# Performance work log

Measured on AMD Instinct MI355X. Metric: run time of the kernel, lower is better.

The kernel has to match this reference:

```python
import jax, jax.numpy as jnp
import numpy as np

B, S, D = 1, 2048, 2048
H, KV, HD = 16, 4, 128
E, TOPK, F = 8, 2, 2048
THETA = 500000.0
CLIP = 8.0
EPS = 1e-5


def setup_inputs() -> dict:
    key = jax.random.key(0)
    ks = jax.random.split(key, 8)
    sc = 0.02
    return {
        "hidden_states": jax.random.normal(ks[0], (B, S, D), jnp.float32),
        "position_ids": jnp.arange(S, dtype=jnp.int64)[None, :].repeat(B, axis=0),
        "ln1_w": jnp.ones((D,), jnp.float32),
        "ln2_w": jnp.ones((D,), jnp.float32),
        "wqkv": jax.random.normal(ks[1], (D, (H + 2 * KV) * HD), jnp.float32) * sc,
        "wo": jax.random.normal(ks[2], (H * HD, D), jnp.float32) * sc,
        "router_w": jax.random.normal(ks[3], (E, D), jnp.float32) * sc,
        "w1": jax.random.normal(ks[4], (E, D, F), jnp.float32) * sc,
        "v1": jax.random.normal(ks[5], (E, D, F), jnp.float32) * sc,
        "w2": jax.random.normal(ks[6], (E, F, D), jnp.float32) * sc,
    }


def _layernorm(x, w):
    mu = jnp.mean(x, axis=-1, keepdims=True)
    var = jnp.mean((x - mu) ** 2, axis=-1, keepdims=True)
    return (x - mu) * jax.lax.rsqrt(var + EPS) * w


def _rotate_half(x):
    x1, x2 = jnp.split(x, 2, axis=-1)
    return jnp.concatenate([-x2, x1], axis=-1)


def _rope(pos):
    inv_freq = 1.0 / (THETA ** (jnp.arange(0, HD, 2, dtype=jnp.float32) / HD))
    ang = pos.astype(jnp.float32)[..., None] * inv_freq  # [B,S,HD/2]
    ang = jnp.concatenate([ang, ang], axis=-1)  # [B,S,HD]
    return jnp.cos(ang)[:, None], jnp.sin(ang)[:, None]  # [B,1,S,HD]


def _forward(hidden_states, position_ids, ln1_w, ln2_w, wqkv, wo, router_w, w1, v1, w2):
    x = hidden_states
    # --- attention sublayer ---
    h = _layernorm(x, ln1_w)
    qkv = jnp.clip(h @ wqkv, -CLIP, CLIP)  # [B,S,(H+2KV)*HD]
    q, k, v = jnp.split(qkv, [H * HD, (H + KV) * HD], axis=-1)
    q = q.reshape(B, S, H, HD).transpose(0, 2, 1, 3)   # [B,H,S,HD]
    k = k.reshape(B, S, KV, HD).transpose(0, 2, 1, 3)  # [B,KV,S,HD]
    v = v.reshape(B, S, KV, HD).transpose(0, 2, 1, 3)
    cos, sin = _rope(position_ids)
    q = q * cos + _rotate_half(q) * sin
    k = k * cos + _rotate_half(k) * sin
    rep = H // KV
    k = jnp.repeat(k, rep, axis=1)  # [B,H,S,HD]
    v = jnp.repeat(v, rep, axis=1)
    scores = jnp.einsum("bhqd,bhkd->bhqk", q, k) / np.sqrt(HD).astype(np.float32)
    causal = jnp.tril(jnp.ones((S, S), bool))
    scores = jnp.where(causal, scores, jnp.finfo(scores.dtype).min)
    probs = jax.nn.softmax(scores, axis=-1)
    attn = jnp.einsum("bhqk,bhkd->bhqd", probs, v)
    attn = attn.transpose(0, 2, 1, 3).reshape(B, S, H * HD) @ wo
    x = x + attn
    # --- MoE FFN sublayer ---
    h = _layernorm(x, ln2_w).reshape(B * S, D)  # [T,D]
    logits = h @ router_w.T                      # [T,E]
    rp = jax.nn.softmax(logits, axis=-1)
    top_w, top_i = jax.lax.top_k(rp, TOPK)       # [T,K]
    top_w = top_w / jnp.sum(top_w, axis=-1, keepdims=True)
    T = B * S
    gate = jnp.zeros((T, E), h.dtype).at[jnp.arange(T)[:, None], top_i].add(top_w)
    g = jax.nn.silu(jnp.einsum("td,edf->tef", h, w1)) * jnp.einsum("td,edf->tef", h, v1)
    y = jnp.einsum("tef,efd,te->td", g, w2, gate)
    x = x + y.reshape(B, S, D)
    return x


def reference(hidden_states, position_ids, ln1_w, ln2_w, wqkv, wo, router_w, w1, v1, w2):
    return _forward(hidden_states, position_ids, ln1_w, ln2_w, wqkv, wo, router_w, w1, v1, w2)
```

## Files before the change

kernel.cpp:

```cpp
#include <hip/hip_runtime.h>

#define S_LEN 2048
#define DMODEL 2048
#define NH 16
#define NKV 4
#define HD 128
#define NE 8
#define FF 2048
#define QKV_N 3072

typedef __attribute__((ext_vector_type(8))) short short8;
typedef __attribute__((ext_vector_type(4))) float f32x4;

__device__ inline unsigned short f2bf(float f) {
  unsigned int u = __builtin_bit_cast(unsigned int, f);
  u += 0x7fffu + ((u >> 16) & 1u);
  return (unsigned short)(u >> 16);
}
__device__ inline float bf2f(unsigned short h) {
  unsigned int u = ((unsigned int)h) << 16;
  return __builtin_bit_cast(float, u);
}
__device__ inline void split2(float v, unsigned short& h, unsigned short& l) {
  h = f2bf(v);
  l = f2bf(v - bf2f(h));
}


__device__ inline void gload16(const void* g, void* l) {
  __builtin_amdgcn_global_load_lds((const __attribute__((address_space(1))) unsigned int*)g,
                                   (__attribute__((address_space(3))) unsigned int*)l,
                                   16, 0, 0);
}
__device__ inline void stageB_chunk(const unsigned short* __restrict__ chunk,
                                    unsigned short* __restrict__ lds) {
  int w = threadIdx.x >> 6, l = threadIdx.x & 63;
  const unsigned short* s = chunk + w * 1024 + l * 8;
  unsigned short* d = lds + w * 1024;
  gload16(s, d);
  gload16(s + 512, d + 512);
}

#define WVM0   asm volatile("s_waitcnt vmcnt(0)" ::: "memory")
#define WVM4   asm volatile("s_waitcnt vmcnt(4)" ::: "memory")
#define WVM6   asm volatile("s_waitcnt vmcnt(6)" ::: "memory")
#define WVM8   asm volatile("s_waitcnt vmcnt(8)" ::: "memory")
#define WVM12  asm volatile("s_waitcnt vmcnt(12)" ::: "memory")
#define WAIT_ALL  asm volatile("s_waitcnt vmcnt(0) lgkmcnt(0)" ::: "memory")
#define WAIT_LDS  asm volatile("s_waitcnt lgkmcnt(0)" ::: "memory")
#define SCHEDBAR  __builtin_amdgcn_sched_barrier(0)
#define BAR       __builtin_amdgcn_s_barrier()


__device__ inline void mma16(const unsigned short* As, const unsigned short* Bs,
                             int wr, int wc, f32x4 acc[4][4]) {
  int l = threadIdx.x & 63;
  int lr = l & 15, lg = l >> 4;
  int qoff = ((lg ^ ((lr ^ (lr >> 2)) & 3)) << 3);
  short8 a[4], b[4];
#pragma unroll
  for (int m = 0; m < 4; m++)
    a[m] = *(const short8*)(As + (wr + m * 16 + lr) * 32 + qoff);
#pragma unroll
  for (int n = 0; n < 4; n++)
    b[n] = *(const short8*)(Bs + (wc + n * 16 + lr) * 32 + qoff);
#pragma unroll
  for (int m = 0; m < 4; m++)
#pragma unroll
    for (int n = 0; n < 4; n++)
      acc[m][n] = __builtin_amdgcn_mfma_f32_16x16x32_bf16(a[m], b[n], acc[m][n], 0, 0, 0);
}

__device__ inline void mma16_dualB(const unsigned short* As, const unsigned short* Bs1,
                                   const unsigned short* Bs2, int wr, int wc,
                                   f32x4 acc1[4][4], f32x4 acc2[4][4]) {
  int l = threadIdx.x & 63;
  int lr = l & 15, lg = l >> 4;
  int qoff = ((lg ^ ((lr ^ (lr >> 2)) & 3)) << 3);
  short8 a[4], b1[4], b2[4];
#pragma unroll
  for (int m = 0; m < 4; m++)
    a[m] = *(const short8*)(As + (wr + m * 16 + lr) * 32 + qoff);
#pragma unroll
  for (int n = 0; n < 4; n++) {
    b1[n] = *(const short8*)(Bs1 + (wc + n * 16 + lr) * 32 + qoff);
    b2[n] = *(const short8*)(Bs2 + (wc + n * 16 + lr) * 32 + qoff);
  }
#pragma unroll
  for (int m = 0; m < 4; m++)
#pragma unroll
    for (int n = 0; n < 4; n++) {
      acc1[m][n] = __builtin_amdgcn_mfma_f32_16x16x32_bf16(a[m], b1[n], acc1[m][n], 0, 0, 0);
      acc2[m][n] = __builtin_amdgcn_mfma_f32_16x16x32_bf16(a[m], b2[n], acc2[m][n], 0, 0, 0);
    }
}

__device__ inline void mma16_split_reg(const unsigned short* Ash, const unsigned short* Asl,
                                       const unsigned short* Bsh, const unsigned short* Bsl,
                                       int wr, int wc, f32x4 acc[4][4]) {
  int l = threadIdx.x & 63;
  int lr = l & 15, lg = l >> 4;
  int qoff = ((lg ^ ((lr ^ (lr >> 2)) & 3)) << 3);
  short8 ah[4], al[4], bh[4], bl[4];
#pragma unroll
  for (int m = 0; m < 4; m++) {
    ah[m] = *(const short8*)(Ash + (wr + m * 16 + lr) * 32 + qoff);
    al[m] = *(const short8*)(Asl + (wr + m * 16 + lr) * 32 + qoff);
  }
#pragma unroll
  for (int n = 0; n < 4; n++) {
    bh[n] = *(const short8*)(Bsh + (wc + n * 16 + lr) * 32 + qoff);
    bl[n] = *(const short8*)(Bsl + (wc + n * 16 + lr) * 32 + qoff);
  }
#pragma unroll
  for (int m = 0; m < 4; m++)
#pragma unroll
    for (int n = 0; n < 4; n++) {
      acc[m][n] = __builtin_amdgcn_mfma_f32_16x16x32_bf16(ah[m], bh[n], acc[m][n], 0, 0, 0);
      acc[m][n] = __builtin_amdgcn_mfma_f32_16x16x32_bf16(ah[m], bl[n], acc[m][n], 0, 0, 0);
      acc[m][n] = __builtin_amdgcn_mfma_f32_16x16x32_bf16(al[m], bh[n], acc[m][n], 0, 0, 0);
    }
}


__global__ __launch_bounds__(256) void k_pack1(const float* __restrict__ src, long ld,
                                               long zs, int nc,
                                               unsigned short* __restrict__ dst) {
  __shared__ float tile[32][132];
  const float* Sp = src + (long)blockIdx.z * zs;
  int c = blockIdx.x, t = threadIdx.x;
  for (int i = 0; i < 4; i++) {
    int kt = blockIdx.y * 4 + i;
    long k0 = (long)kt * 32, n0 = (long)c * 128;
    {
      int k = t >> 3, nn = (t & 7) * 16;
      const float4* p = (const float4*)(Sp + (k0 + k) * ld + n0 + nn);
#pragma unroll
      for (int j = 0; j < 4; j++) *(float4*)&tile[k][nn + j * 4] = p[j];
    }
    __syncthreads();
    size_t cbase = ((size_t)(blockIdx.z * nc + c) * 64 + kt) * 4096;
#pragma unroll
    for (int uu = 0; uu < 2; uu++) {
      int u = t * 2 + uu;
      int n = u >> 2, qp = u & 3;
      int q = qp ^ ((n ^ (n >> 2)) & 3);
      unsigned short hb[8] __attribute__((aligned(16)));
#pragma unroll
      for (int j = 0; j < 8; j++) hb[j] = f2bf(tile[8 * q + j][n]);
      *(uint4*)(dst + cbase + u * 8) = *(const uint4*)hb;
    }
    __syncthreads();
  }
}

__global__ __launch_bounds__(256) void k_pack2(const float* __restrict__ src, long ld,
                                               long zs, int nc,
                                               unsigned short* __restrict__ dh,
                                               unsigned short* __restrict__ dl) {
  __shared__ float tile[32][132];
  const float* Sp = src + (long)blockIdx.z * zs;
  int c = blockIdx.x, t = threadIdx.x;
  for (int i = 0; i < 4; i++) {
    int kt = blockIdx.y * 4 + i;
    long k0 = (long)kt * 32, n0 = (long)c * 128;
    {
      int k = t >> 3, nn = (t & 7) * 16;
      const float4* p = (const float4*)(Sp + (k0 + k) * ld + n0 + nn);
#pragma unroll
      for (int j = 0; j < 4; j++) *(float4*)&tile[k][nn + j * 4] = p[j];
    }
    __syncthreads();
    size_t cbase = ((size_t)(blockIdx.z * nc + c) * 64 + kt) * 4096;
#pragma unroll
    for (int uu = 0; uu < 2; uu++) {
      int u = t * 2 + uu;
      int n = u >> 2, qp = u & 3;
      int q = qp ^ ((n ^ (n >> 2)) & 3);
      unsigned short hb[8] __attribute__((aligned(16)));
      unsigned short lb[8] __attribute__((aligned(16)));
#pragma unroll
      for (int j = 0; j < 8; j++) split2(tile[8 * q + j][n], hb[j], lb[j]);
      *(uint4*)(dh + cbase + u * 8) = *(const uint4*)hb;
      *(uint4*)(dl + cbase + u * 8) = *(const uint4*)lb;
    }
    __syncthreads();
  }
}


__global__ __launch_bounds__(256) void k_qkv_s(const unsigned short* __restrict__ APh,
                                               const unsigned short* __restrict__ APl,
                                               const unsigned short* __restrict__ BPh,
                                               const unsigned short* __restrict__ BPl,
                                               float* __restrict__ C) {
  __shared__ unsigned short Ash[2 * 4096], Asl[2 * 4096], Bsh[2 * 4096], Bsl[2 * 4096];
  size_t ab = (size_t)blockIdx.y * 64 * 4096;
  size_t cb = (size_t)blockIdx.x * 64 * 4096;
  int w = threadIdx.x >> 6;
  int wr = (w >> 1) * 64, wc = (w & 1) * 64;
  stageB_chunk(APh + ab, Ash);
  stageB_chunk(APl + ab, Asl);
  stageB_chunk(BPh + cb, Bsh);
  stageB_chunk(BPl + cb, Bsl);
  WAIT_ALL;
  BAR;
  f32x4 acc[4][4] = {};
  for (int kt = 0; kt < 64; kt++) {
    int cur = (kt & 1) << 12, nxt = 4096 - cur;
    if (kt + 1 < 64) {
      size_t o = (size_t)(kt + 1) * 4096;
      stageB_chunk(APh + ab + o, Ash + nxt);
      stageB_chunk(APl + ab + o, Asl + nxt);
      stageB_chunk(BPh + cb + o, Bsh + nxt);
      stageB_chunk(BPl + cb + o, Bsl + nxt);
    }
    SCHEDBAR;
    mma16_split_reg(Ash + cur, Asl + cur, Bsh + cur, Bsl + cur, wr, wc, acc);
    SCHEDBAR;
    WAIT_ALL;
    BAR;
  }
  int row0 = blockIdx.y * 128, col0 = blockIdx.x * 128;
  int l = threadIdx.x & 63;
  int er = wr + ((l >> 4) << 2), ec = wc + (l & 15);
#pragma unroll
  for (int m = 0; m < 4; m++)
#pragma unroll
    for (int n = 0; n < 4; n++)
#pragma unroll
      for (int r = 0; r < 4; r++) {
        float v = acc[m][n][r];
        v = fminf(fmaxf(v, -8.f), 8.f);
        C[(size_t)(row0 + er + m * 16 + r) * QKV_N + col0 + ec + n * 16] = v;
      }
}

__global__ __launch_bounds__(256) void k_wo_s(const unsigned short* __restrict__ APh,
                                              const unsigned short* __restrict__ APl,
                                              const unsigned short* __restrict__ BPh,
                                              const unsigned short* __restrict__ BPl,
                                              const float* __restrict__ resid,
                                              float* __restrict__ x1) {
  __shared__ unsigned short Ash[2 * 4096], Asl[2 * 4096], Bsh[2 * 4096], Bsl[2 * 4096];
  size_t ab = (size_t)blockIdx.y * 64 * 4096;
  size_t cb = (size_t)blockIdx.x * 64 * 4096;
  int w = threadIdx.x >> 6;
  int wr = (w >> 1) * 64, wc = (w & 1) * 64;
  stageB_chunk(APh + ab, Ash);
  stageB_chunk(APl + ab, Asl);
  stageB_chunk(BPh + cb, Bsh);
  stageB_chunk(BPl + cb, Bsl);
  WAIT_ALL;
  BAR;
  f32x4 acc[4][4] = {};
  for (int kt = 0; kt < 64; kt++) {
    int cur = (kt & 1) << 12, nxt = 4096 - cur;
    if (kt + 1 < 64) {
      size_t o = (size_t)(kt + 1) * 4096;
      stageB_chunk(APh + ab + o, Ash + nxt);
      stageB_chunk(APl + ab + o, Asl + nxt);
      stageB_chunk(BPh + cb + o, Bsh + nxt);
      stageB_chunk(BPl + cb + o, Bsl + nxt);
    }
    SCHEDBAR;
    mma16_split_reg(Ash + cur, Asl + cur, Bsh + cur, Bsl + cur, wr, wc, acc);
    SCHEDBAR;
    WAIT_ALL;
    BAR;
  }
  int row0 = blockIdx.y * 128, col0 = blockIdx.x * 128;
  int l = threadIdx.x & 63;
  int er = wr + ((l >> 4) << 2), ec = wc + (l & 15);
#pragma unroll
  for (int m = 0; m < 4; m++)
#pragma unroll
    for (int n = 0; n < 4; n++)
#pragma unroll
      for (int r = 0; r < 4; r++) {
        size_t idx = (size_t)(row0 + er + m * 16 + r) * DMODEL + col0 + ec + n * 16;
        x1[idx] = resid[idx] + acc[m][n][r];
      }
}


__global__ __launch_bounds__(128) void k_flash(const unsigned short* __restrict__ qh,
                                               const unsigned short* __restrict__ ql,
                                               const unsigned short* __restrict__ kPh,
                                               const unsigned short* __restrict__ kPl,
                                               const unsigned short* __restrict__ vPh,
                                               const unsigned short* __restrict__ vPl,
                                               unsigned short* __restrict__ atPh,
                                               unsigned short* __restrict__ atPl) {
  int bid = blockIdx.x;
  int h = (bid & 7) | ((bid >> 8) << 3);
  int rt = (bid >> 3) & 31;
  int kv = h >> 2;
  int ntiles = (rt >> 1) + 1;
  __shared__ float Pds[2][32 * 132];
  int t = threadIdx.x;
  int w = t >> 6, l = t & 63;
  int lr = l & 15, lg = l >> 4;
  int qoff = ((lg ^ ((lr ^ (lr >> 2)) & 3)) << 3);
  int wrow0 = rt * 64 + w * 32;
  const unsigned short* Qbh = qh + (size_t)h * S_LEN * HD;
  const unsigned short* Qbl = ql + (size_t)h * S_LEN * HD;
  const unsigned short* Kch = kPh + (size_t)kv * 64 * 4096;
  const unsigned short* Kcl = kPl + (size_t)kv * 64 * 4096;
  const unsigned short* Vch = vPh + (size_t)kv * 64 * 4096;
  const unsigned short* Vcl = vPl + (size_t)kv * 64 * 4096;
  float* Pw = &Pds[w][0];
  float mrun[2][4], lrun[2][4];
  f32x4 Oc[2][8];
#pragma unroll
  for (int m = 0; m < 2; m++)
#pragma unroll
    for (int r = 0; r < 4; r++) { mrun[m][r] = -3.4e38f; lrun[m][r] = 0.f; }
#pragma unroll
  for (int m = 0; m < 2; m++)
#pragma unroll
    for (int n = 0; n < 8; n++)
#pragma unroll
      for (int r = 0; r < 4; r++) Oc[m][n][r] = 0.f;
  const float scale = 0.08838834764831845f;

  for (int kt = 0; kt < ntiles; kt++) {
    f32x4 Sa[2][8];
#pragma unroll
    for (int m = 0; m < 2; m++)
#pragma unroll
      for (int n = 0; n < 8; n++)
#pragma unroll
        for (int r = 0; r < 4; r++) Sa[m][n][r] = 0.f;
#pragma unroll
    for (int kst = 0; kst < 4; kst++) {
      short8 qfh[2], qfl[2];
#pragma unroll
      for (int m = 0; m < 2; m++) {
        size_t o = (size_t)(wrow0 + m * 16 + lr) * HD + kst * 32 + lg * 8;
        qfh[m] = *(const short8*)(Qbh + o);
        qfl[m] = *(const short8*)(Qbl + o);
      }
      const unsigned short* Kh = Kch + (size_t)(kt * 4 + kst) * 4096;
      const unsigned short* Kl = Kcl + (size_t)(kt * 4 + kst) * 4096;
      short8 bh[8], bl[8];
#pragma unroll
      for (int n = 0; n < 8; n++) {
        bh[n] = *(const short8*)(Kh + (n * 16 + lr) * 32 + qoff);
        bl[n] = *(const short8*)(Kl + (n * 16 + lr) * 32 + qoff);
      }
#pragma unroll
      for (int m = 0; m < 2; m++)
#pragma unroll
        for (int n = 0; n < 8; n++) {
          Sa[m][n] = __builtin_amdgcn_mfma_f32_16x16x32_bf16(qfh[m], bh[n], Sa[m][n], 0, 0, 0);
          Sa[m][n] = __builtin_amdgcn_mfma_f32_16x16x32_bf16(qfh[m], bl[n], Sa[m][n], 0, 0, 0);
          Sa[m][n] = __builtin_amdgcn_mfma_f32_16x16x32_bf16(qfl[m], bh[n], Sa[m][n], 0, 0, 0);
        }
    }
#pragma unroll
    for (int m = 0; m < 2; m++)
#pragma unroll
      for (int r = 0; r < 4; r++) {
        int row = wrow0 + m * 16 + lg * 4 + r;
        float mx = mrun[m][r];
#pragma unroll
        for (int n = 0; n < 8; n++) {
          float v = Sa[m][n][r] * scale;
          int col = kt * 128 + n * 16 + lr;
          v = (col <= row) ? v : -3.4e38f;
          Sa[m][n][r] = v;
          mx = fmaxf(mx, v);
        }
        mx = fmaxf(mx, __shfl_xor(mx, 1));
        mx = fmaxf(mx, __shfl_xor(mx, 2));
        mx = fmaxf(mx, __shfl_xor(mx, 4));
        mx = fmaxf(mx, __shfl_xor(mx, 8));
        float al_ = expf(mrun[m][r] - mx);
        float sum = 0.f;
#pragma unroll
        for (int n = 0; n < 8; n++) {
          float v = Sa[m][n][r];
          float e = (v > -1.0e37f) ? expf(v - mx) : 0.f;
          Sa[m][n][r] = e;
          sum += e;
        }
        sum += __shfl_xor(sum, 1);
        sum += __shfl_xor(sum, 2);
        sum += __shfl_xor(sum, 4);
        sum += __shfl_xor(sum, 8);
        lrun[m][r] = lrun[m][r] * al_ + sum;
        mrun[m][r] = mx;
#pragma unroll
        for (int n = 0; n < 8; n++) Oc[m][n][r] *= al_;
      }
    WAIT_LDS;
    SCHEDBAR;
#pragma unroll
    for (int m = 0; m < 2; m++)
#pragma unroll
      for (int n = 0; n < 8; n++)
#pragma unroll
        for (int r = 0; r < 4; r++)
          Pw[(m * 16 + lg * 4 + r) * 132 + n * 16 + lr] = Sa[m][n][r];
    WAIT_LDS;
    SCHEDBAR;
#pragma unroll
    for (int kst = 0; kst < 4; kst++) {
      const unsigned short* Vh = Vch + (size_t)(kt * 4 + kst) * 4096;
      const unsigned short* Vl = Vcl + (size_t)(kt * 4 + kst) * 4096;
      short8 bh[8], bl[8];
#pragma unroll
      for (int n = 0; n < 8; n++) {
        bh[n] = *(const short8*)(Vh + (n * 16 + lr) * 32 + qoff);
        bl[n] = *(const short8*)(Vl + (n * 16 + lr) * 32 + qoff);
      }
#pragma unroll
      for (int m = 0; m < 2; m++) {
        const float* pp = &Pw[(m * 16 + lr) * 132 + kst * 32 + lg * 8];
        unsigned short ahb[8] __attribute__((aligned(16)));
        unsigned short alb[8] __attribute__((aligned(16)));
#pragma unroll
        for (int j = 0; j < 8; j++) split2(pp[j], ahb[j], alb[j]);
        short8 ah = *(const short8*)ahb;
        short8 al_ = *(const short8*)alb;
#pragma unroll
        for (int n = 0; n < 8; n++) {
          Oc[m][n] = __builtin_amdgcn_mfma_f32_16x16x32_bf16(ah, bh[n], Oc[m][n], 0, 0, 0);
          Oc[m][n] = __builtin_amdgcn_mfma_f32_16x16x32_bf16(ah, bl[n], Oc[m][n], 0, 0, 0);
          Oc[m][n] = __builtin_amdgcn_mfma_f32_16x16x32_bf16(al_, bh[n], Oc[m][n], 0, 0, 0);
        }
      }
    }
  }
#pragma unroll
  for (int m = 0; m < 2; m++)
#pragma unroll
    for (int r = 0; r < 4; r++) {
      int row = wrow0 + m * 16 + lg * 4 + r;
      int rtc = row >> 7, rl = row & 127;
      int sr = (rl ^ (rl >> 2)) & 3;
      float lv = lrun[m][r];
#pragma unroll
      for (int n = 0; n < 8; n++) {
        int col = h * HD + n * 16 + lr;
        size_t off = ((size_t)(rtc * 64 + (col >> 5))) * 4096 + rl * 32 +
                     ((((col & 31) >> 3) ^ sr) << 3) + (col & 7);
        unsigned short hh, ll;
        split2(Oc[m][n][r] / lv, hh, ll);
        atPh[off] = hh;
        atPl[off] = ll;
      }
    }
}


__global__ __launch_bounds__(256) void k_moe1f(const unsigned short* __restrict__ h2b,
                                               const int* __restrict__ ptok,
                                               const unsigned short* __restrict__ wPa,
                                               const unsigned short* __restrict__ wPb,
                                               const int* __restrict__ meta,
                                               unsigned short* __restrict__ g) {
  int ty = blockIdx.y;
  if (ty >= meta[25]) return;
  int tt = meta[26 + ty];
  int e = tt & 7, m0 = tt >> 3;
  int nvalid = min(128, meta[e] - m0);
  const unsigned short* B1 = wPa + (size_t)(e * 16 + blockIdx.x) * 64 * 4096;
  const unsigned short* B2 = wPb + (size_t)(e * 16 + blockIdx.x) * 64 * 4096;
  __shared__ unsigned short L[3][3][4096];
  int w = threadIdx.x >> 6;
  int lid = threadIdx.x & 63;
  int wr = (w >> 1) * 64, wc = (w & 1) * 64;
  int r0 = w * 32 + (lid >> 2);
  int qx = lid & 3;
  int s0 = (r0 ^ (r0 >> 2)) & 3;
  long pb = (long)meta[16 + e] + m0;
  int tk0 = ptok[pb + min(r0, nvalid - 1)];
  int tk1 = ptok[pb + min(r0 + 16, nvalid - 1)];
  const unsigned short* a0 = h2b + (size_t)tk0 * DMODEL + ((qx ^ s0) << 3);
  const unsigned short* a1 = h2b + (size_t)tk1 * DMODEL + ((qx ^ s0) << 3);
#pragma unroll
  for (int p = 0; p < 3; p++) {
    size_t o = (size_t)p * 4096;
    unsigned short* dA = &L[p][0][0] + w * 1024;
    gload16(a0 + p * 32, dA);
    gload16(a1 + p * 32, dA + 512);
    stageB_chunk(B1 + o, &L[p][1][0]);
    stageB_chunk(B2 + o, &L[p][2][0]);
  }
  WVM12;
  BAR;
  f32x4 acc1[4][4] = {}, acc2[4][4] = {};
  int cur = 0;
  for (int kt = 0; kt < 64; kt++) {
    SCHEDBAR;
    mma16_dualB(&L[cur][0][0], &L[cur][1][0], &L[cur][2][0], wr, wc, acc1, acc2);
    SCHEDBAR;
    BAR;
    if (kt + 3 < 64) {
      size_t o = (size_t)(kt + 3) * 4096;
      unsigned short* dA = &L[cur][0][0] + w * 1024;
      gload16(a0 + (kt + 3) * 32, dA);
      gload16(a1 + (kt + 3) * 32, dA + 512);
      stageB_chunk(B1 + o, &L[cur][1][0]);
      stageB_chunk(B2 + o, &L[cur][2][0]);
      WVM12;
    } else if (kt + 3 == 64) {
      WVM6;
    } else {
      WVM0;
    }
    BAR;
    cur = (cur == 2) ? 0 : cur + 1;
  }
  int l = threadIdx.x & 63;
  int er = wr + ((l >> 4) << 2), ec = wc + (l & 15);
  int ktf0 = blockIdx.x * 4;
#pragma unroll
  for (int m = 0; m < 4; m++)
#pragma unroll
    for (int n = 0; n < 4; n++)
#pragma unroll
      for (int r = 0; r < 4; r++) {
        int rl = er + m * 16 + r;
        int cc = ec + n * 16;
        float a = acc1[m][n][r];
        float s = a / (1.f + expf(-a));
        unsigned short val = (rl < nvalid) ? f2bf(s * acc2[m][n][r]) : (unsigned short)0;
        int srl = (rl ^ (rl >> 2)) & 3;
        g[((size_t)(ty * 64 + ktf0 + (cc >> 5))) * 4096 + rl * 32 +
          ((((cc & 31) >> 3) ^ srl) << 3) + (cc & 7)] = val;
      }
}

__global__ __launch_bounds__(256) void k_moe2(const unsigned short* __restrict__ gP,
                                              const unsigned short* __restrict__ wP,
                                              const int* __restrict__ ptok,
                                              const float* __restrict__ pw,
                                              const int* __restrict__ meta,
                                              float* __restrict__ out) {
  int ty = blockIdx.y;
  if (ty >= meta[25]) return;
  int tt = meta[26 + ty];
  int e = tt & 7, m0 = tt >> 3;
  int nvalid = min(128, meta[e] - m0);
  long pbase = (long)meta[16 + e] + m0;
  int kc = blockIdx.z;
  const unsigned short* Ab = gP + ((size_t)ty * 64 + kc * 32) * 4096;
  const unsigned short* Bb = wP + ((size_t)(e * 16 + blockIdx.x) * 64 + kc * 32) * 4096;
  __shared__ unsigned short L[3][2][4096];
  int w = threadIdx.x >> 6;
  int wr = (w >> 1) * 64, wc = (w & 1) * 64;
#pragma unroll
  for (int p = 0; p < 3; p++) {
    size_t o = (size_t)p * 4096;
    stageB_chunk(Ab + o, &L[p][0][0]);
    stageB_chunk(Bb + o, &L[p][1][0]);
  }
  WVM8;
  BAR;
  f32x4 acc[4][4] = {};
  int cur = 0;
  for (int kt = 0; kt < 32; kt++) {
    SCHEDBAR;
    mma16(&L[cur][0][0], &L[cur][1][0], wr, wc, acc);
    SCHEDBAR;
    BAR;
    if (kt + 3 < 32) {
      size_t o = (size_t)(kt + 3) * 4096;
      stageB_chunk(Ab + o, &L[cur][0][0]);
      stageB_chunk(Bb + o, &L[cur][1][0]);
      WVM8;
    } else if (kt + 3 == 32) {
      WVM4;
    } else {
      WVM0;
    }
    BAR;
    cur = (cur == 2) ? 0 : cur + 1;
  }
  int col0 = blockIdx.x * 128;
  int l = threadIdx.x & 63;
  int er = wr + ((l >> 4) << 2), ec = wc + (l & 15);
#pragma unroll
  for (int m = 0; m < 4; m++)
#pragma unroll
    for (int n = 0; n < 4; n++)
#pragma unroll
      for (int r = 0; r < 4; r++) {
        int rl = er + m * 16 + r;
        if (rl < nvalid) {
          long p = pbase + rl;
          int tk = ptok[p];
          atomicAdd(&out[(size_t)tk * DMODEL + col0 + ec + n * 16], acc[m][n][r] * pw[p]);
        }
      }
}


__global__ __launch_bounds__(256) void k_ln(const float* __restrict__ x,
                                            const float* __restrict__ w,
                                            unsigned short* __restrict__ obh,
                                            unsigned short* __restrict__ obl,
                                            float* __restrict__ of, int mode) {
  int row = blockIdx.x;
  const float* xr = x + (size_t)row * DMODEL;
  float s = 0.f, ss = 0.f;
  for (int c = threadIdx.x; c < DMODEL; c += 256) {
    float v = xr[c];
    s += v; ss += v * v;
  }
#pragma unroll
  for (int o = 32; o; o >>= 1) { s += __shfl_down(s, o); ss += __shfl_down(ss, o); }
  __shared__ float rs[4], rss[4], mu_s, inv_s;
  int wid = threadIdx.x >> 6;
  if ((threadIdx.x & 63) == 0) { rs[wid] = s; rss[wid] = ss; }
  __syncthreads();
  if (threadIdx.x == 0) {
    float S1 = rs[0] + rs[1] + rs[2] + rs[3];
    float S2 = rss[0] + rss[1] + rss[2] + rss[3];
    float mu = S1 / DMODEL;
    mu_s = mu;
    inv_s = rsqrtf(S2 / DMODEL - mu * mu + 1e-5f);
  }
  __syncthreads();
  float mu = mu_s, inv = inv_s;
  int rt = row >> 7, rl = row & 127;
  int sw = (rl ^ (rl >> 2)) & 3;
  for (int c = threadIdx.x; c < DMODEL; c += 256) {
    float v = (xr[c] - mu) * inv * w[c];
    unsigned short hh, ll;
    split2(v, hh, ll);
    if (mode) {
      size_t off = ((size_t)(rt * 64 + (c >> 5))) * 4096 + rl * 32 +
                   ((((c & 31) >> 3) ^ sw) << 3) + (c & 7);
      obh[off] = hh;
      obl[off] = ll;
    } else {
      obh[(size_t)row * DMODEL + c] = hh;
      obl[(size_t)row * DMODEL + c] = ll;
      of[(size_t)row * DMODEL + c] = v;
    }
  }
}

__global__ void k_rope2(const float* __restrict__ qkv, unsigned short* __restrict__ qh,
                        unsigned short* __restrict__ ql, unsigned short* __restrict__ kPh,
                        unsigned short* __restrict__ kPl) {
  int t = blockIdx.x;
  int d = threadIdx.x;
  float pf = (float)pow(500000.0, (double)d * (1.0 / 64.0));
  float invf = 1.0f / pf;
  float ang = (float)t * invf;
  float cs = (float)cos((double)ang);
  float sn = (float)sin((double)ang);
  const float* row = qkv + (size_t)t * QKV_N;
  unsigned short hh, ll;
#pragma unroll
  for (int hq = 0; hq < NH; hq++) {
    float a = row[hq * HD + d], b = row[hq * HD + d + 64];
    size_t base = ((size_t)hq * S_LEN + t) * HD;
    split2(a * cs - b * sn, hh, ll); qh[base + d] = hh; ql[base + d] = ll;
    split2(b * cs + a * sn, hh, ll); qh[base + d + 64] = hh; ql[base + d + 64] = ll;
  }
  int tt2 = t >> 7, rl2 = t & 127;
  int s2 = (rl2 ^ (rl2 >> 2)) & 3;
#pragma unroll
  for (int kv = 0; kv < NKV; kv++) {
    float a = row[NH * HD + kv * HD + d], b = row[NH * HD + kv * HD + d + 64];
    float o0 = a * cs - b * sn;
    float o1 = b * cs + a * sn;
#pragma unroll
    for (int half = 0; half < 2; half++) {
      int col = d + half * 64;
      float v = half ? o1 : o0;
      size_t off = ((size_t)(kv * 64 + tt2 * 4 + (col >> 5))) * 4096 + rl2 * 32 +
                   ((((col & 31) >> 3) ^ s2) << 3) + (col & 7);
      split2(v, hh, ll);
      kPh[off] = hh;
      kPl[off] = ll;
    }
  }
}

__global__ __launch_bounds__(256) void k_router(const float* __restrict__ h2,
                                                const float* __restrict__ rw,
                                                int* __restrict__ topi,
                                                float* __restrict__ topw,
                                                int* __restrict__ cnt) {
  int t = blockIdx.x;
  __shared__ float hs[DMODEL];
  __shared__ float lg[NE];
  for (int c = threadIdx.x; c < DMODEL; c += 256) hs[c] = h2[(size_t)t * DMODEL + c];
  __syncthreads();
  int grp = threadIdx.x >> 5;
  int ln = threadIdx.x & 31;
  float p = 0.f;
  for (int c = ln; c < DMODEL; c += 32) p += hs[c] * rw[(size_t)grp * DMODEL + c];
#pragma unroll
  for (int o = 16; o; o >>= 1) p += __shfl_down(p, o, 32);
  if (ln == 0) lg[grp] = p;
  __syncthreads();
  if (threadIdx.x == 0) {
    float l0 = -3.4e38f; int i0 = 0;
    for (int e = 0; e < NE; e++)
      if (lg[e] > l0) { l0 = lg[e]; i0 = e; }
    float l1 = -3.4e38f; int i1 = 0;
    for (int e = 0; e < NE; e++)
      if (e != i0 && lg[e] > l1) { l1 = lg[e]; i1 = e; }
    float z = expf(l1 - l0);
    topi[t * 2] = i0; topi[t * 2 + 1] = i1;
    topw[t * 2] = 1.f / (1.f + z); topw[t * 2 + 1] = z / (1.f + z);
    atomicAdd(&cnt[i0], 1);
    atomicAdd(&cnt[i1], 1);
  }
}

__global__ void k_scan(int* __restrict__ meta) {
  if (threadIdx.x == 0 && blockIdx.x == 0) {
    int o = 0, nt = 0;
    for (int e = 0; e < NE; e++) {
      meta[16 + e] = o;
      for (int m0 = 0; m0 < meta[e]; m0 += 128) meta[26 + nt++] = (m0 << 3) | e;
      o += meta[e];
    }
    meta[24] = o;
    meta[25] = nt;
  }
}

__global__ void k_fill(const int* __restrict__ topi, const float* __restrict__ topw,
                       int* __restrict__ meta, int* __restrict__ ptok,
                       float* __restrict__ pw) {
  int t = blockIdx.x * blockDim.x + threadIdx.x;
  if (t >= S_LEN) return;
#pragma unroll
  for (int j = 0; j < 2; j++) {
    int e = topi[t * 2 + j];
    int p = atomicAdd(&meta[8 + e], 1);
    ptok[meta[16 + e] + p] = t;
    pw[meta[16 + e] + p] = topw[t * 2 + j];
  }
}


extern "C" void kernel_launch(void* const* d_in, const int* in_sizes, int n_in,
                              void* d_out, int out_size, void* d_ws, size_t ws_size,
                              hipStream_t stream) {
  (void)in_sizes; (void)n_in; (void)out_size; (void)ws_size;
  const float* x = (const float*)d_in[0];
  const float* ln1w = (const float*)d_in[2];
  const float* ln2w = (const float*)d_in[3];
  const float* wqkv = (const float*)d_in[4];
  const float* wo = (const float*)d_in[5];
  const float* rw = (const float*)d_in[6];
  const float* w1 = (const float*)d_in[7];
  const float* v1 = (const float*)d_in[8];
  const float* w2 = (const float*)d_in[9];
  float* out = (float*)d_out;

  char* wsb = (char*)d_ws;
  const size_t MiB = 1u << 20;
  unsigned short* h1Ph = (unsigned short*)(wsb + 0 * MiB);
  unsigned short* h1Pl = (unsigned short*)(wsb + 8 * MiB);
  float* qkvb = (float*)(wsb + 16 * MiB);
  unsigned short* qh = (unsigned short*)(wsb + 40 * MiB);
  unsigned short* ql = (unsigned short*)(wsb + 48 * MiB);
  unsigned short* vPh = (unsigned short*)(wsb + 60 * MiB);
  unsigned short* vPl = (unsigned short*)(wsb + 62 * MiB);
  unsigned short* kPh = (unsigned short*)(wsb + 64 * MiB);
  unsigned short* kPl = (unsigned short*)(wsb + 66 * MiB);
  unsigned short* atPh = (unsigned short*)(wsb + 68 * MiB);
  unsigned short* atPl = (unsigned short*)(wsb + 76 * MiB);
  unsigned short* wqkvPh = (unsigned short*)(wsb + 84 * MiB);
  unsigned short* wqkvPl = (unsigned short*)(wsb + 96 * MiB);
  unsigned short* woPh = (unsigned short*)(wsb + 108 * MiB);
  unsigned short* woPl = (unsigned short*)(wsb + 116 * MiB);
  unsigned short* h2b = (unsigned short*)(wsb + 0 * MiB);
  unsigned short* h2lo = (unsigned short*)(wsb + 8 * MiB);
  unsigned short* g = (unsigned short*)(wsb + 16 * MiB);
  float* h2f = (float*)(wsb + 40 * MiB);
  unsigned short* wPa = (unsigned short*)(wsb + 40 * MiB);
  unsigned short* wPb = (unsigned short*)(wsb + 104 * MiB);
  char* small = wsb + 168 * MiB;
  int* topi = (int*)small;
  float* topw = (float*)(small + 16384);
  int* ptok = (int*)(small + 32768);
  float* pw = (float*)(small + 49152);
  int* meta = (int*)(small + 65536);

  k_pack2<<<dim3(QKV_N / 128, 16, 1), 256, 0, stream>>>(wqkv, QKV_N, 0, QKV_N / 128,
                                                        wqkvPh, wqkvPl);
  k_pack2<<<dim3(DMODEL / 128, 16, 1), 256, 0, stream>>>(wo, DMODEL, 0, DMODEL / 128,
                                                         woPh, woPl);

  k_ln<<<S_LEN, 256, 0, stream>>>(x, ln1w, h1Ph, h1Pl, (float*)nullptr, 1);
  k_qkv_s<<<dim3(QKV_N / 128, S_LEN / 128), 256, 0, stream>>>(h1Ph, h1Pl, wqkvPh, wqkvPl,
                                                              qkvb);
  k_rope2<<<S_LEN, 64, 0, stream>>>(qkvb, qh, ql, kPh, kPl);
  k_pack2<<<dim3(1, 16, NKV), 256, 0, stream>>>(qkvb + (NH + NKV) * HD, QKV_N, HD, 1,
                                                vPh, vPl);
  k_flash<<<512, 128, 0, stream>>>(qh, ql, kPh, kPl, vPh, vPl, atPh, atPl);
  k_wo_s<<<dim3(16, 16), 256, 0, stream>>>(atPh, atPl, woPh, woPl, x, out);

  k_ln<<<S_LEN, 256, 0, stream>>>(out, ln2w, h2b, h2lo, h2f, 0);
  hipMemsetAsync(meta, 0, 512, stream);
  k_router<<<S_LEN, 256, 0, stream>>>(h2f, rw, topi, topw, meta);
  k_scan<<<1, 64, 0, stream>>>(meta);
  k_fill<<<8, 256, 0, stream>>>(topi, topw, meta, ptok, pw);
  k_pack1<<<dim3(16, 16, NE), 256, 0, stream>>>(w1, FF, (long)DMODEL * FF, 16, wPa);
  k_pack1<<<dim3(16, 16, NE), 256, 0, stream>>>(v1, FF, (long)DMODEL * FF, 16, wPb);
  k_moe1f<<<dim3(16, 40), 256, 0, stream>>>(h2b, ptok, wPa, wPb, meta, g);
  k_pack1<<<dim3(16, 16, NE), 256, 0, stream>>>(w2, DMODEL, (long)FF * DMODEL, 16, wPa);
  k_moe2<<<dim3(16, 40, 2), 256, 0, stream>>>(g, wPa, ptok, pw, meta, out);
}
```

Before: 912.1 us.

## Deepen split-bf16 GEMM prefetch to two stages with partial vmcnt waits

Result: no change. 909.7 us (-0.3%).

```diff
diff --git a/kernel.cpp b/kernel.cpp
--- a/kernel.cpp
+++ b/kernel.cpp
@@ -199,26 +199,34 @@
   size_t cb = (size_t)blockIdx.x * 64 * 4096;
   int w = threadIdx.x >> 6;
   int wr = (w >> 1) * 64, wc = (w & 1) * 64;
-  stageB_chunk(APh + ab, Ash);
-  stageB_chunk(APl + ab, Asl);
-  stageB_chunk(BPh + cb, Bsh);
-  stageB_chunk(BPl + cb, Bsl);
-  WAIT_ALL;
+#pragma unroll
+  for (int p = 0; p < 2; p++) {
+    size_t o = (size_t)p * 4096;
+    int b = p << 12;
+    stageB_chunk(APh + ab + o, Ash + b);
+    stageB_chunk(APl + ab + o, Asl + b);
+    stageB_chunk(BPh + cb + o, Bsh + b);
+    stageB_chunk(BPl + cb + o, Bsl + b);
+  }
+  WVM8;
   BAR;
   f32x4 acc[4][4] = {};
   for (int kt = 0; kt < 64; kt++) {
-    int cur = (kt & 1) << 12, nxt = 4096 - cur;
-    if (kt + 1 < 64) {
-      size_t o = (size_t)(kt + 1) * 4096;
-      stageB_chunk(APh + ab + o, Ash + nxt);
-      stageB_chunk(APl + ab + o, Asl + nxt);
-      stageB_chunk(BPh + cb + o, Bsh + nxt);
-      stageB_chunk(BPl + cb + o, Bsl + nxt);
-    }
+    int cur = (kt & 1) << 12;
     SCHEDBAR;
     mma16_split_reg(Ash + cur, Asl + cur, Bsh + cur, Bsl + cur, wr, wc, acc);
     SCHEDBAR;
-    WAIT_ALL;
+    BAR;
+    if (kt + 2 < 64) {
+      size_t o = (size_t)(kt + 2) * 4096;
+      stageB_chunk(APh + ab + o, Ash + cur);
+      stageB_chunk(APl + ab + o, Asl + cur);
+      stageB_chunk(BPh + cb + o, Bsh + cur);
+      stageB_chunk(BPl + cb + o, Bsl + cur);
+      WVM8;
+    } else {
+      WVM0;
+    }
     BAR;
   }
   int row0 = blockIdx.y * 128, col0 = blockIdx.x * 128;
@@ -247,26 +255,34 @@
   size_t cb = (size_t)blockIdx.x * 64 * 4096;
   int w = threadIdx.x >> 6;
   int wr = (w >> 1) * 64, wc = (w & 1) * 64;
-  stageB_chunk(APh + ab, Ash);
-  stageB_chunk(APl + ab, Asl);
-  stageB_chunk(BPh + cb, Bsh);
-  stageB_chunk(BPl + cb, Bsl);
-  WAIT_ALL;
+#pragma unroll
+  for (int p = 0; p < 2; p++) {
+    size_t o = (size_t)p * 4096;
+    int b = p << 12;
+    stageB_chunk(APh + ab + o, Ash + b);
+    stageB_chunk(APl + ab + o, Asl + b);
+    stageB_chunk(BPh + cb + o, Bsh + b);
+    stageB_chunk(BPl + cb + o, Bsl + b);
+  }
+  WVM8;
   BAR;
   f32x4 acc[4][4] = {};
   for (int kt = 0; kt < 64; kt++) {
-    int cur = (kt & 1) << 12, nxt = 4096 - cur;
-    if (kt + 1 < 64) {
-      size_t o = (size_t)(kt + 1) * 4096;
-      stageB_chunk(APh + ab + o, Ash + nxt);
-      stageB_chunk(APl + ab + o, Asl + nxt);
-      stageB_chunk(BPh + cb + o, Bsh + nxt);
-      stageB_chunk(BPl + cb + o, Bsl + nxt);
-    }
+    int cur = (kt & 1) << 12;
     SCHEDBAR;
     mma16_split_reg(Ash + cur, Asl + cur, Bsh + cur, Bsl + cur, wr, wc, acc);
     SCHEDBAR;
-    WAIT_ALL;
+    BAR;
+    if (kt + 2 < 64) {
+      size_t o = (size_t)(kt + 2) * 4096;
+      stageB_chunk(APh + ab + o, Ash + cur);
+      stageB_chunk(APl + ab + o, Asl + cur);
+      stageB_chunk(BPh + cb + o, Bsh + cur);
+      stageB_chunk(BPl + cb + o, Bsl + cur);
+      WVM8;
+    } else {
+      WVM0;
+    }
     BAR;
   }
   int row0 = blockIdx.y * 128, col0 = blockIdx.x * 128;
@@ -639,8 +655,8 @@
       obl[off] = ll;
     } else {
       obh[(size_t)row * DMODEL + c] = hh;
-      obl[(size_t)row * DMODEL + c] = ll;
-      of[(size_t)row * DMODEL + c] = v;
+      if (obl) obl[(size_t)row * DMODEL + c] = ll;
+      if (of) of[(size_t)row * DMODEL + c] = v;
     }
   }
 }
@@ -778,7 +794,6 @@
   unsigned short* woPh = (unsigned short*)(wsb + 108 * MiB);
   unsigned short* woPl = (unsigned short*)(wsb + 116 * MiB);
   unsigned short* h2b = (unsigned short*)(wsb + 0 * MiB);
-  unsigned short* h2lo = (unsigned short*)(wsb + 8 * MiB);
   unsigned short* g = (unsigned short*)(wsb + 16 * MiB);
   float* h2f = (float*)(wsb + 40 * MiB);
   unsigned short* wPa = (unsigned short*)(wsb + 40 * MiB);
@@ -804,7 +819,7 @@
   k_flash<<<512, 128, 0, stream>>>(qh, ql, kPh, kPl, vPh, vPl, atPh, atPl);
   k_wo_s<<<dim3(16, 16), 256, 0, stream>>>(atPh, atPl, woPh, woPl, x, out);
 
-  k_ln<<<S_LEN, 256, 0, stream>>>(out, ln2w, h2b, h2lo, h2f, 0);
+  k_ln<<<S_LEN, 256, 0, stream>>>(out, ln2w, h2b, (unsigned short*)nullptr, h2f, 0);
   hipMemsetAsync(meta, 0, 512, stream);
   k_router<<<S_LEN, 256, 0, stream>>>(h2f, rw, topi, topw, meta);
   k_scan<<<1, 64, 0, stream>>>(meta);
```
